# Optimization experiments

Hardware: AMD Instinct MI355X
Metric: run time of the kernel (lower is better)

The kernel has to match this reference:

```python
import jax, jax.numpy as jnp
import numpy as np

N = 50000          # nodes
E = 800000         # edges
D_IN = 96          # node_encoding_length
D = 128            # hidden_encoding_length (args.node_encoding)
B = 512            # graphs in batch
MPNN_STEPS = 4
S2S_STEPS = 3


def setup_inputs() -> dict:
    key = jax.random.key(0)
    ks = jax.random.split(key, 12)
    x = jax.random.normal(ks[0], (N, D_IN), dtype=jnp.float32)
    edge_index = jax.random.randint(ks[1], (2, E), 0, N, dtype=jnp.int64)
    batch = jnp.sort(jax.random.randint(ks[2], (N,), 0, B, dtype=jnp.int64))
    s_in = 1.0 / np.sqrt(D_IN)
    W_in = jax.random.uniform(ks[3], (D, D_IN), jnp.float32, -s_in, s_in)
    b_in = jax.random.uniform(ks[4], (D,), jnp.float32, -s_in, s_in)
    s_l = 1.0 / np.sqrt(D)
    W_ih = jax.random.uniform(ks[5], (4 * D, 2 * D), jnp.float32, -s_l, s_l)
    W_hh = jax.random.uniform(ks[6], (4 * D, D), jnp.float32, -s_l, s_l)
    b_ih = jax.random.uniform(ks[7], (4 * D,), jnp.float32, -s_l, s_l)
    b_hh = jax.random.uniform(ks[8], (4 * D,), jnp.float32, -s_l, s_l)
    s_p = 1.0 / np.sqrt(2 * D)
    W_pred = jax.random.uniform(ks[9], (1, 2 * D), jnp.float32, -s_p, s_p)
    b_pred = jax.random.uniform(ks[10], (1,), jnp.float32, -s_p, s_p)
    return {"x": x, "edge_index": edge_index, "batch": batch,
            "W_in": W_in, "b_in": b_in, "W_ih": W_ih, "W_hh": W_hh,
            "b_ih": b_ih, "b_hh": b_hh, "W_pred": W_pred, "b_pred": b_pred}


def _forward(x, edge_index, batch, W_in, b_in, W_ih, W_hh, b_ih, b_hh, W_pred, b_pred):
    # input layer + relu
    h = jax.nn.relu(x @ W_in.T + b_in)                      # [N, D]
    src, dst = edge_index[0], edge_index[1]
    # precompute in-degree for mean aggregation (clamped to 1 like scatter-mean)
    deg = jax.ops.segment_sum(jnp.ones((E,), h.dtype), dst, num_segments=N)
    deg = jnp.maximum(deg, 1.0)[:, None]                    # [N, 1]
    # MPNN: gather x_j at src, mean-aggregate at dst, update x=(x+msg)/2
    for _ in range(MPNN_STEPS):
        msg = jax.ops.segment_sum(h[src], dst, num_segments=N) / deg
        h = (h + msg) * 0.5
    # Set2Set readout
    d = h.shape[1]
    q_star = jnp.zeros((B, 2 * d), h.dtype)
    hh = jnp.zeros((B, d), h.dtype)
    cc = jnp.zeros((B, d), h.dtype)
    for _ in range(S2S_STEPS):
        gates = q_star @ W_ih.T + b_ih + hh @ W_hh.T + b_hh  # [B, 4d]
        i_g, f_g, g_g, o_g = jnp.split(gates, 4, axis=-1)
        cc = jax.nn.sigmoid(f_g) * cc + jax.nn.sigmoid(i_g) * jnp.tanh(g_g)
        hh = jax.nn.sigmoid(o_g) * jnp.tanh(cc)
        q = hh                                               # [B, d]
        e = jnp.sum(h * q[batch], axis=-1)                   # [N]
        e_max = jax.ops.segment_max(e, batch, num_segments=B)
        a = jnp.exp(e - e_max[batch])
        a_sum = jax.ops.segment_sum(a, batch, num_segments=B)
        a = a / (a_sum[batch] + 1e-16)
        r = jax.ops.segment_sum(a[:, None] * h, batch, num_segments=B)  # [B, d]
        q_star = jnp.concatenate([q, r], axis=-1)
    return q_star @ W_pred.T + b_pred                        # [B, 1]


def reference(x, edge_index, batch, W_in, b_in, W_ih, W_hh, b_ih, b_hh, W_pred, b_pred):
    return _forward(x, edge_index, batch, W_in, b_in, W_ih, W_hh, b_ih, b_hh, W_pred, b_pred)
```

## Files before the change

### kernel.cpp

```cpp
#include <hip/hip_runtime.h>
#include <math.h>
#include <float.h>

#define N_NODES 50000
#define N_EDGES 800000
#define D_INP   96
#define D_HID   128
#define N_B     512
#define CAP     64
#define XS_LD   100

typedef __attribute__((ext_vector_type(4))) _Float16 half4;
typedef __attribute__((ext_vector_type(8))) _Float16 half8;

__global__ __launch_bounds__(256) void k_ingemm_prep(
        const float* __restrict__ x,
        const float* __restrict__ W_in,
        const float* __restrict__ b_in,
        const float* __restrict__ W_ih,
        const float* __restrict__ W_hh,
        const int* __restrict__ batch,
        _Float16* __restrict__ h16,
        float* __restrict__ Wt2,
        int* __restrict__ cnt,
        int* __restrict__ seg_ptr) {
    int gid = (blockIdx.y * gridDim.x + blockIdx.x) * 256 + threadIdx.x;
    if (gid < N_NODES) {
        cnt[gid] = 0;
        int n = gid;
        int bc = batch[n];
        int bp = (n == 0) ? -1 : batch[n - 1];
        for (int b = bp + 1; b <= bc; b++) seg_ptr[b] = n;
        if (n == N_NODES - 1)
            for (int b = bc + 1; b <= N_B; b++) seg_ptr[b] = N_NODES;
    }
    if (gid < 256 * 512) {
        int k = gid / 512, g = gid % 512;
        float v = W_ih[g * 256 + k];
        if (k < 128) v += W_hh[g * 128 + k];
        Wt2[gid] = v;
    }

    __shared__ __align__(16) float xs[64 * XS_LD];
    __shared__ __align__(16) float ws[96 * 64];
    int n0 = blockIdx.x * 64;
    int d0 = blockIdx.y * 64;
    int tid = threadIdx.x;
    for (int j = tid; j < 64 * 96 / 4; j += 256) {
        int row = (j * 4) / 96, col = (j * 4) % 96;
        int node = n0 + row;
        float4 v = make_float4(0.f, 0.f, 0.f, 0.f);
        if (node < N_NODES) v = *(const float4*)&x[(size_t)node * 96 + col];
        *(float4*)&xs[row * XS_LD + col] = v;
    }
    for (int i = tid; i < 96 * 64; i += 256) {
        int k = i >> 6, dd = i & 63;
        ws[i] = W_in[(size_t)(d0 + dd) * 96 + k];
    }
    __syncthreads();
    int tn = tid / 16;
    int td = tid % 16;
    float acc[4][4] = {};
    for (int k0 = 0; k0 < 96; k0 += 4) {
        float4 w0 = *(float4*)&ws[(k0 + 0) * 64 + td * 4];
        float4 w1 = *(float4*)&ws[(k0 + 1) * 64 + td * 4];
        float4 w2 = *(float4*)&ws[(k0 + 2) * 64 + td * 4];
        float4 w3 = *(float4*)&ws[(k0 + 3) * 64 + td * 4];
#pragma unroll
        for (int j = 0; j < 4; j++) {
            float4 xv = *(float4*)&xs[(tn * 4 + j) * XS_LD + k0];
            acc[j][0] += xv.x * w0.x + xv.y * w1.x + xv.z * w2.x + xv.w * w3.x;
            acc[j][1] += xv.x * w0.y + xv.y * w1.y + xv.z * w2.y + xv.w * w3.y;
            acc[j][2] += xv.x * w0.z + xv.y * w1.z + xv.z * w2.z + xv.w * w3.z;
            acc[j][3] += xv.x * w0.w + xv.y * w1.w + xv.z * w2.w + xv.w * w3.w;
        }
    }
    float4 bb = *(const float4*)&b_in[d0 + td * 4];
#pragma unroll
    for (int j = 0; j < 4; j++) {
        int node = n0 + tn * 4 + j;
        if (node < N_NODES) {
            half4 s;
            s.x = (_Float16)fmaxf(acc[j][0] + bb.x, 0.f);
            s.y = (_Float16)fmaxf(acc[j][1] + bb.y, 0.f);
            s.z = (_Float16)fmaxf(acc[j][2] + bb.z, 0.f);
            s.w = (_Float16)fmaxf(acc[j][3] + bb.w, 0.f);
            *(half4*)&h16[(size_t)node * D_HID + d0 + td * 4] = s;
        }
    }
}

__global__ void k_bucket8(const int* __restrict__ src, const int* __restrict__ dst,
                          int* __restrict__ cnt, unsigned short* __restrict__ esrc) {
    int chunk = blockIdx.x >> 3;
    int part  = blockIdx.x & 7;
    int e = chunk * 256 + threadIdx.x;
    if (e < N_EDGES) {
        int d = dst[e];
        if ((d & 7) == part) {
            int p = atomicAdd(&cnt[d], 1);
            if (p < CAP) esrc[(size_t)d * CAP + p] = (unsigned short)src[e];
        }
    }
}

__global__ __launch_bounds__(256) void k_mpnn(const _Float16* __restrict__ hin16,
                                              _Float16* __restrict__ hout16,
                                              const int* __restrict__ cnt,
                                              const unsigned short* __restrict__ esrc) {
    int g = threadIdx.x >> 4;
    int l = threadIdx.x & 15;
    int n = blockIdx.x * 16 + g;
    if (n >= N_NODES) return;
    int deg = cnt[n];
    int len = min(deg, CAP);
    const unsigned short* row = &esrc[(size_t)n * CAP];
    float a0[8] = {}, a1[8] = {}, a2[8] = {}, a3[8] = {};
    int i = 0;
    for (; i + 4 <= len; i += 4) {
        int e0 = row[i + 0];
        int e1 = row[i + 1];
        int e2 = row[i + 2];
        int e3 = row[i + 3];
        half8 v0 = *(const half8*)&hin16[(size_t)e0 * 128 + l * 8];
        half8 v1 = *(const half8*)&hin16[(size_t)e1 * 128 + l * 8];
        half8 v2 = *(const half8*)&hin16[(size_t)e2 * 128 + l * 8];
        half8 v3 = *(const half8*)&hin16[(size_t)e3 * 128 + l * 8];
#pragma unroll
        for (int c = 0; c < 8; c++) {
            a0[c] += (float)v0[c];
            a1[c] += (float)v1[c];
            a2[c] += (float)v2[c];
            a3[c] += (float)v3[c];
        }
    }
    for (; i < len; i++) {
        int e0 = row[i];
        half8 v0 = *(const half8*)&hin16[(size_t)e0 * 128 + l * 8];
#pragma unroll
        for (int c = 0; c < 8; c++) a0[c] += (float)v0[c];
    }
#pragma unroll
    for (int c = 0; c < 8; c++) a0[c] += a1[c] + a2[c] + a3[c];
    float invd = 1.0f / (float)max(deg, 1);
    half8 sv = *(const half8*)&hin16[(size_t)n * 128 + l * 8];
    half8 s;
#pragma unroll
    for (int c = 0; c < 8; c++)
        s[c] = (_Float16)(((float)sv[c] + a0[c] * invd) * 0.5f);
    *(half8*)&hout16[(size_t)n * 128 + l * 8] = s;
}

__device__ __forceinline__ float sigmoidf_(float v) { return 1.0f / (1.0f + expf(-v)); }

__global__ __launch_bounds__(1024) void k_s2s2(const float* __restrict__ Wt2,
                                               const float* __restrict__ b_ih,
                                               const float* __restrict__ b_hh,
                                               const _Float16* __restrict__ h16,
                                               const int* __restrict__ seg_ptr,
                                               const float* __restrict__ W_pred,
                                               const float* __restrict__ b_pred,
                                               float* __restrict__ out) {
    __shared__ __align__(16) float in_s[2 * 256];
    __shared__ __align__(16) float c_s[2 * 128];
    __shared__ __align__(16) float bias_s[512];
    __shared__ __align__(16) float gpart_s[2][2][512];
    __shared__ float smax_s[2][16];
    __shared__ float ssum_s[2][16];
    __shared__ __align__(16) float sr_s[2][16][128];

    int t = threadIdx.x;
    if (t < 512) {
        in_s[t] = 0.f;
        bias_s[t] = b_ih[t] + b_hh[t];
    }
    if (t < 256) c_s[t] = 0.f;

    int gate = t & 511;
    int kh   = t >> 9;
    int row  = t >> 9;
    int loc  = t & 511;
    int gq   = loc >> 5;
    int l    = t & 31;
    int b    = blockIdx.x * 2 + row;
    int s0 = seg_ptr[b], s1 = seg_ptr[b + 1];

    for (int step = 0; step < 3; step++) {
        __syncthreads();
        {
            float acc0 = 0.f, acc1 = 0.f;
            int k0 = kh * 128;
#pragma unroll 8
            for (int k = k0; k < k0 + 128; k++) {
                float w = Wt2[k * 512 + gate];
                acc0 += in_s[k] * w;
                acc1 += in_s[256 + k] * w;
            }
            gpart_s[kh][0][gate] = acc0;
            gpart_s[kh][1][gate] = acc1;
        }
        __syncthreads();
        if (t < 256) {
            int r2 = t >> 7, ff = t & 127;
            float ig = gpart_s[0][r2][ff]       + gpart_s[1][r2][ff]       + bias_s[ff];
            float fg = gpart_s[0][r2][128 + ff] + gpart_s[1][r2][128 + ff] + bias_s[128 + ff];
            float gg = gpart_s[0][r2][256 + ff] + gpart_s[1][r2][256 + ff] + bias_s[256 + ff];
            float og = gpart_s[0][r2][384 + ff] + gpart_s[1][r2][384 + ff] + bias_s[384 + ff];
            float c = sigmoidf_(fg) * c_s[r2 * 128 + ff] + sigmoidf_(ig) * tanhf(gg);
            c_s[r2 * 128 + ff] = c;
            in_s[r2 * 256 + ff] = sigmoidf_(og) * tanhf(c);
        }
        __syncthreads();
        float4 q = *(float4*)&in_s[row * 256 + l * 4];
        float Ma = -INFINITY, sa = 0.f;
        float Mb = -INFINITY, sb = 0.f;
        float4 ra = make_float4(0.f, 0.f, 0.f, 0.f);
        float4 rb = make_float4(0.f, 0.f, 0.f, 0.f);
        for (int n = s0 + gq; n < s1; n += 32) {
            {
                half4 h4 = *(const half4*)&h16[(size_t)n * 128 + l * 4];
                float4 hv = make_float4((float)h4.x, (float)h4.y, (float)h4.z, (float)h4.w);
                float d = hv.x * q.x + hv.y * q.y + hv.z * q.z + hv.w * q.w;
                for (int m = 16; m >= 1; m >>= 1) d += __shfl_xor(d, m, 64);
                float nM = fmaxf(Ma, d);
                float sc = expf(Ma - nM);
                float a = expf(d - nM);
                sa = sa * sc + a;
                ra.x = ra.x * sc + a * hv.x;
                ra.y = ra.y * sc + a * hv.y;
                ra.z = ra.z * sc + a * hv.z;
                ra.w = ra.w * sc + a * hv.w;
                Ma = nM;
            }
            int n2 = n + 16;
            if (n2 < s1) {
                half4 h4 = *(const half4*)&h16[(size_t)n2 * 128 + l * 4];
                float4 hv = make_float4((float)h4.x, (float)h4.y, (float)h4.z, (float)h4.w);
                float d = hv.x * q.x + hv.y * q.y + hv.z * q.z + hv.w * q.w;
                for (int m = 16; m >= 1; m >>= 1) d += __shfl_xor(d, m, 64);
                float nM = fmaxf(Mb, d);
                float sc = expf(Mb - nM);
                float a = expf(d - nM);
                sb = sb * sc + a;
                rb.x = rb.x * sc + a * hv.x;
                rb.y = rb.y * sc + a * hv.y;
                rb.z = rb.z * sc + a * hv.z;
                rb.w = rb.w * sc + a * hv.w;
                Mb = nM;
            }
        }
        float M = fmaxf(Ma, Mb);
        float wa = (Ma > -INFINITY) ? expf(Ma - M) : 0.f;
        float wb = (Mb > -INFINITY) ? expf(Mb - M) : 0.f;
        float asum = sa * wa + sb * wb;
        float4 racc;
        racc.x = ra.x * wa + rb.x * wb;
        racc.y = ra.y * wa + rb.y * wb;
        racc.z = ra.z * wa + rb.z * wb;
        racc.w = ra.w * wa + rb.w * wb;
        if (l == 0) { smax_s[row][gq] = M; ssum_s[row][gq] = asum; }
        *(float4*)&sr_s[row][gq][l * 4] = racc;
        __syncthreads();
        if (gq == 0) {
            float Mx = -INFINITY;
#pragma unroll
            for (int i = 0; i < 16; i++) Mx = fmaxf(Mx, smax_s[row][i]);
            float4 o = make_float4(0.f, 0.f, 0.f, 0.f);
            if (Mx > -INFINITY) {
                float tot = 0.f;
                float4 osum = make_float4(0.f, 0.f, 0.f, 0.f);
#pragma unroll
                for (int i = 0; i < 16; i++) {
                    float wi = expf(smax_s[row][i] - Mx);
                    tot += ssum_s[row][i] * wi;
                    float4 ri = *(float4*)&sr_s[row][i][l * 4];
                    osum.x += ri.x * wi; osum.y += ri.y * wi;
                    osum.z += ri.z * wi; osum.w += ri.w * wi;
                }
                float inv = 1.0f / (tot + 1e-16f);
                o.x = osum.x * inv; o.y = osum.y * inv;
                o.z = osum.z * inv; o.w = osum.w * inv;
            }
            *(float4*)&in_s[row * 256 + 128 + l * 4] = o;
            if (step == 2) {
                float4 wq = *(const float4*)&W_pred[l * 4];
                float4 wr = *(const float4*)&W_pred[128 + l * 4];
                float d = q.x * wq.x + q.y * wq.y + q.z * wq.z + q.w * wq.w
                        + o.x * wr.x + o.y * wr.y + o.z * wr.z + o.w * wr.w;
                for (int m = 16; m >= 1; m >>= 1) d += __shfl_xor(d, m, 64);
                if (l == 0) out[b] = d + b_pred[0];
            }
        }
    }
}

extern "C" void kernel_launch(void* const* d_in, const int* in_sizes, int n_in,
                              void* d_out, int out_size, void* d_ws, size_t ws_size,
                              hipStream_t stream) {
    const float* x      = (const float*)d_in[0];
    const int*   edge   = (const int*)d_in[1];
    const int*   batch  = (const int*)d_in[2];
    const float* W_in   = (const float*)d_in[3];
    const float* b_in   = (const float*)d_in[4];
    const float* W_ih   = (const float*)d_in[5];
    const float* W_hh   = (const float*)d_in[6];
    const float* b_ih   = (const float*)d_in[7];
    const float* b_hh   = (const float*)d_in[8];
    const float* W_pred = (const float*)d_in[9];
    const float* b_pred = (const float*)d_in[10];
    float* out = (float*)d_out;

    const int* src = edge;
    const int* dst = edge + N_EDGES;

    float* f = (float*)d_ws;
    _Float16* g0 = (_Float16*)f;          f += (size_t)N_NODES * D_HID / 2;
    _Float16* g1 = (_Float16*)f;          f += (size_t)N_NODES * D_HID / 2;
    float* Wt2   = f;                     f += 256 * 512;
    int* ip = (int*)f;
    int* cnt     = ip;                    ip += N_NODES;
    int* seg_ptr = ip;                    ip += N_B + 1 + 3;
    unsigned short* esrc = (unsigned short*)ip;

    k_ingemm_prep<<<dim3((N_NODES + 63) / 64, 2), 256, 0, stream>>>(
        x, W_in, b_in, W_ih, W_hh, batch, g0, Wt2, cnt, seg_ptr);

    k_bucket8<<<((N_EDGES + 255) / 256) * 8, 256, 0, stream>>>(src, dst, cnt, esrc);

    int mb = (N_NODES + 15) / 16;
    k_mpnn<<<mb, 256, 0, stream>>>(g0, g1, cnt, esrc);
    k_mpnn<<<mb, 256, 0, stream>>>(g1, g0, cnt, esrc);
    k_mpnn<<<mb, 256, 0, stream>>>(g0, g1, cnt, esrc);
    k_mpnn<<<mb, 256, 0, stream>>>(g1, g0, cnt, esrc);

    k_s2s2<<<N_B / 2, 1024, 0, stream>>>(Wt2, b_ih, b_hh, g0, seg_ptr,
                                         W_pred, b_pred, out);
}
```

Baseline: 321.6 us.

## Fuse final MPNN step into Set2Set kernel with per-graph LDS node cache

```diff
diff --git a/kernel.cpp b/kernel.cpp
--- a/kernel.cpp
+++ b/kernel.cpp
@@ -9,43 +9,37 @@
 #define N_B     512
 #define CAP     64
 #define XS_LD   100
+#define HLN     160
+#define TAILCAP 64
 
 typedef __attribute__((ext_vector_type(4))) _Float16 half4;
 typedef __attribute__((ext_vector_type(8))) _Float16 half8;
 
-__global__ __launch_bounds__(256) void k_ingemm_prep(
-        const float* __restrict__ x,
-        const float* __restrict__ W_in,
-        const float* __restrict__ b_in,
-        const float* __restrict__ W_ih,
-        const float* __restrict__ W_hh,
-        const int* __restrict__ batch,
-        _Float16* __restrict__ h16,
-        float* __restrict__ Wt2,
-        int* __restrict__ cnt,
-        int* __restrict__ seg_ptr) {
+__global__ __launch_bounds__(256) void k_ingemm(const float* __restrict__ x,
+                                                const float* __restrict__ W_in,
+                                                const float* __restrict__ b_in,
+                                                _Float16* __restrict__ h16,
+                                                int* __restrict__ cnt) {
     int gid = (blockIdx.y * gridDim.x + blockIdx.x) * 256 + threadIdx.x;
-    if (gid < N_NODES) {
-        cnt[gid] = 0;
-        int n = gid;
-        int bc = batch[n];
-        int bp = (n == 0) ? -1 : batch[n - 1];
-        for (int b = bp + 1; b <= bc; b++) seg_ptr[b] = n;
-        if (n == N_NODES - 1)
-            for (int b = bc + 1; b <= N_B; b++) seg_ptr[b] = N_NODES;
-    }
-    if (gid < 256 * 512) {
-        int k = gid / 512, g = gid % 512;
-        float v = W_ih[g * 256 + k];
-        if (k < 128) v += W_hh[g * 128 + k];
-        Wt2[gid] = v;
-    }
+    if (gid < N_NODES) cnt[gid] = 0;
 
     __shared__ __align__(16) float xs[64 * XS_LD];
     __shared__ __align__(16) float ws[96 * 64];
     int n0 = blockIdx.x * 64;
     int d0 = blockIdx.y * 64;
     int tid = threadIdx.x;
+
+    for (int i = tid; i < 64 * 24; i += 256) {
+        int row = i / 24, c4 = i % 24;
+        float4 v = *(const float4*)&W_in[(size_t)(d0 + row) * 96 + c4 * 4];
+        *(float4*)&xs[row * XS_LD + c4 * 4] = v;
+    }
+    __syncthreads();
+    for (int i = tid; i < 96 * 64; i += 256) {
+        int k = i >> 6, dd = i & 63;
+        ws[i] = xs[dd * XS_LD + k];
+    }
+    __syncthreads();
     for (int j = tid; j < 64 * 96 / 4; j += 256) {
         int row = (j * 4) / 96, col = (j * 4) % 96;
         int node = n0 + row;
@@ -53,11 +47,8 @@
         if (node < N_NODES) v = *(const float4*)&x[(size_t)node * 96 + col];
         *(float4*)&xs[row * XS_LD + col] = v;
     }
-    for (int i = tid; i < 96 * 64; i += 256) {
-        int k = i >> 6, dd = i & 63;
-        ws[i] = W_in[(size_t)(d0 + dd) * 96 + k];
-    }
     __syncthreads();
+
     int tn = tid / 16;
     int td = tid % 16;
     float acc[4][4] = {};
@@ -91,7 +82,26 @@
 }
 
 __global__ void k_bucket8(const int* __restrict__ src, const int* __restrict__ dst,
-                          int* __restrict__ cnt, unsigned short* __restrict__ esrc) {
+                          const int* __restrict__ batch,
+                          const float* __restrict__ W_ih,
+                          const float* __restrict__ W_hh,
+                          int* __restrict__ cnt, unsigned short* __restrict__ esrc,
+                          int* __restrict__ seg_ptr, float* __restrict__ Wt2) {
+    int gid = blockIdx.x * 256 + threadIdx.x;
+    if (gid < N_NODES) {
+        int n = gid;
+        int bc = batch[n];
+        int bp = (n == 0) ? -1 : batch[n - 1];
+        for (int b = bp + 1; b <= bc; b++) seg_ptr[b] = n;
+        if (n == N_NODES - 1)
+            for (int b = bc + 1; b <= N_B; b++) seg_ptr[b] = N_NODES;
+    }
+    if (gid < 256 * 512) {
+        int k = gid / 512, g = gid % 512;
+        float v = W_ih[g * 256 + k];
+        if (k < 128) v += W_hh[g * 128 + k];
+        Wt2[gid] = v;
+    }
     int chunk = blockIdx.x >> 3;
     int part  = blockIdx.x & 7;
     int e = chunk * 256 + threadIdx.x;
@@ -153,144 +163,160 @@
 
 __device__ __forceinline__ float sigmoidf_(float v) { return 1.0f / (1.0f + expf(-v)); }
 
-__global__ __launch_bounds__(1024) void k_s2s2(const float* __restrict__ Wt2,
-                                               const float* __restrict__ b_ih,
-                                               const float* __restrict__ b_hh,
-                                               const _Float16* __restrict__ h16,
-                                               const int* __restrict__ seg_ptr,
-                                               const float* __restrict__ W_pred,
-                                               const float* __restrict__ b_pred,
-                                               float* __restrict__ out) {
-    __shared__ __align__(16) float in_s[2 * 256];
-    __shared__ __align__(16) float c_s[2 * 128];
+__global__ __launch_bounds__(512) void k_s2s3(const float* __restrict__ Wt2,
+                                              const float* __restrict__ b_ih,
+                                              const float* __restrict__ b_hh,
+                                              const _Float16* __restrict__ h3,
+                                              const int* __restrict__ cnt,
+                                              const unsigned short* __restrict__ esrc,
+                                              const int* __restrict__ seg_ptr,
+                                              const float* __restrict__ W_pred,
+                                              const float* __restrict__ b_pred,
+                                              _Float16* __restrict__ tail,
+                                              float* __restrict__ out) {
+    __shared__ __align__(16) _Float16 hl[HLN * 128];
+    __shared__ __align__(16) float sr_s[32][128];
+    __shared__ __align__(16) float gates_s[512];
+    __shared__ __align__(16) float in_s[256];
+    __shared__ __align__(16) float c_s[128];
     __shared__ __align__(16) float bias_s[512];
-    __shared__ __align__(16) float gpart_s[2][2][512];
-    __shared__ float smax_s[2][16];
-    __shared__ float ssum_s[2][16];
-    __shared__ __align__(16) float sr_s[2][16][128];
+    __shared__ float smax_s[32];
+    __shared__ float ssum_s[32];
+    __shared__ float red_s[128];
 
     int t = threadIdx.x;
-    if (t < 512) {
-        in_s[t] = 0.f;
-        bias_s[t] = b_ih[t] + b_hh[t];
-    }
-    if (t < 256) c_s[t] = 0.f;
-
-    int gate = t & 511;
-    int kh   = t >> 9;
-    int row  = t >> 9;
-    int loc  = t & 511;
-    int gq   = loc >> 5;
-    int l    = t & 31;
-    int b    = blockIdx.x * 2 + row;
+    int b = blockIdx.x;
+    if (t < 256) in_s[t] = 0.f;
+    if (t < 128) c_s[t] = 0.f;
+    bias_s[t] = b_ih[t] + b_hh[t];
+
     int s0 = seg_ptr[b], s1 = seg_ptr[b + 1];
+    int len = s1 - s0;
+    if (len > HLN + TAILCAP) len = HLN + TAILCAP;
+
+    int grp = t >> 4;
+    int lane = t & 15;
+
+    for (int nl = grp; nl < len; nl += 32) {
+        int n = s0 + nl;
+        int deg = cnt[n];
+        int ln = min(deg, CAP);
+        const unsigned short* row = &esrc[(size_t)n * CAP];
+        float a0[8] = {}, a1[8] = {}, a2[8] = {}, a3[8] = {};
+        int i = 0;
+        for (; i + 4 <= ln; i += 4) {
+            int e0 = row[i + 0];
+            int e1 = row[i + 1];
+            int e2 = row[i + 2];
+            int e3 = row[i + 3];
+            half8 v0 = *(const half8*)&h3[(size_t)e0 * 128 + lane * 8];
+            half8 v1 = *(const half8*)&h3[(size_t)e1 * 128 + lane * 8];
+            half8 v2 = *(const half8*)&h3[(size_t)e2 * 128 + lane * 8];
+            half8 v3 = *(const half8*)&h3[(size_t)e3 * 128 + lane * 8];
+#pragma unroll
+            for (int c = 0; c < 8; c++) {
+                a0[c] += (float)v0[c];
+                a1[c] += (float)v1[c];
+                a2[c] += (float)v2[c];
+                a3[c] += (float)v3[c];
+            }
+        }
+        for (; i < ln; i++) {
+            int e0 = row[i];
+            half8 v0 = *(const half8*)&h3[(size_t)e0 * 128 + lane * 8];
+#pragma unroll
+            for (int c = 0; c < 8; c++) a0[c] += (float)v0[c];
+        }
+#pragma unroll
+        for (int c = 0; c < 8; c++) a0[c] += a1[c] + a2[c] + a3[c];
+        float invd = 1.0f / (float)max(deg, 1);
+        half8 sv = *(const half8*)&h3[(size_t)n * 128 + lane * 8];
+        half8 o16;
+#pragma unroll
+        for (int c = 0; c < 8; c++)
+            o16[c] = (_Float16)(((float)sv[c] + a0[c] * invd) * 0.5f);
+        if (nl < HLN)
+            *(half8*)&hl[nl * 128 + lane * 8] = o16;
+        else
+            *(half8*)&tail[((size_t)b * TAILCAP + (nl - HLN)) * 128 + lane * 8] = o16;
+    }
+    __syncthreads();
 
     for (int step = 0; step < 3; step++) {
+        {
+            float acc = 0.f;
+#pragma unroll 8
+            for (int k = 0; k < 256; k++)
+                acc += in_s[k] * Wt2[k * 512 + t];
+            gates_s[t] = acc + bias_s[t];
+        }
         __syncthreads();
-        {
-            float acc0 = 0.f, acc1 = 0.f;
-            int k0 = kh * 128;
-#pragma unroll 8
-            for (int k = k0; k < k0 + 128; k++) {
-                float w = Wt2[k * 512 + gate];
-                acc0 += in_s[k] * w;
-                acc1 += in_s[256 + k] * w;
+        if (t < 128) {
+            float ig = gates_s[t];
+            float fg = gates_s[128 + t];
+            float gg = gates_s[256 + t];
+            float og = gates_s[384 + t];
+            float c = sigmoidf_(fg) * c_s[t] + sigmoidf_(ig) * tanhf(gg);
+            c_s[t] = c;
+            in_s[t] = sigmoidf_(og) * tanhf(c);
+        }
+        __syncthreads();
+        float qr[8];
+#pragma unroll
+        for (int c = 0; c < 8; c++) qr[c] = in_s[lane * 8 + c];
+        float M = -INFINITY, asum = 0.f;
+        float racc[8] = {};
+        for (int nl = grp; nl < len; nl += 32) {
+            half8 hv;
+            if (nl < HLN) hv = *(const half8*)&hl[nl * 128 + lane * 8];
+            else hv = *(const half8*)&tail[((size_t)b * TAILCAP + (nl - HLN)) * 128 + lane * 8];
+            float hf[8];
+#pragma unroll
+            for (int c = 0; c < 8; c++) hf[c] = (float)hv[c];
+            float d = 0.f;
+#pragma unroll
+            for (int c = 0; c < 8; c++) d += qr[c] * hf[c];
+            d += __shfl_xor(d, 8, 64);
+            d += __shfl_xor(d, 4, 64);
+            d += __shfl_xor(d, 2, 64);
+            d += __shfl_xor(d, 1, 64);
+            float nM = fmaxf(M, d);
+            float sc = expf(M - nM);
+            float a = expf(d - nM);
+            asum = asum * sc + a;
+#pragma unroll
+            for (int c = 0; c < 8; c++) racc[c] = racc[c] * sc + a * hf[c];
+            M = nM;
+        }
+        if (lane == 0) { smax_s[grp] = M; ssum_s[grp] = asum; }
+#pragma unroll
+        for (int c = 0; c < 8; c++) sr_s[grp][lane * 8 + c] = racc[c];
+        __syncthreads();
+        if (t < 128) {
+            float Mx = -INFINITY;
+#pragma unroll
+            for (int g = 0; g < 32; g++) Mx = fmaxf(Mx, smax_s[g]);
+            float o = 0.f;
+            if (Mx > -INFINITY) {
+                float tot = 0.f, osum = 0.f;
+#pragma unroll
+                for (int g = 0; g < 32; g++) {
+                    float w = expf(smax_s[g] - Mx);
+                    tot += ssum_s[g] * w;
+                    osum += sr_s[g][t] * w;
+                }
+                o = osum / (tot + 1e-16f);
             }
-            gpart_s[kh][0][gate] = acc0;
-            gpart_s[kh][1][gate] = acc1;
+            in_s[128 + t] = o;
+            if (step == 2)
+                red_s[t] = in_s[t] * W_pred[t] + o * W_pred[128 + t];
         }
         __syncthreads();
-        if (t < 256) {
-            int r2 = t >> 7, ff = t & 127;
-            float ig = gpart_s[0][r2][ff]       + gpart_s[1][r2][ff]       + bias_s[ff];
-            float fg = gpart_s[0][r2][128 + ff] + gpart_s[1][r2][128 + ff] + bias_s[128 + ff];
-            float gg = gpart_s[0][r2][256 + ff] + gpart_s[1][r2][256 + ff] + bias_s[256 + ff];
-            float og = gpart_s[0][r2][384 + ff] + gpart_s[1][r2][384 + ff] + bias_s[384 + ff];
-            float c = sigmoidf_(fg) * c_s[r2 * 128 + ff] + sigmoidf_(ig) * tanhf(gg);
-            c_s[r2 * 128 + ff] = c;
-            in_s[r2 * 256 + ff] = sigmoidf_(og) * tanhf(c);
-        }
-        __syncthreads();
-        float4 q = *(float4*)&in_s[row * 256 + l * 4];
-        float Ma = -INFINITY, sa = 0.f;
-        float Mb = -INFINITY, sb = 0.f;
-        float4 ra = make_float4(0.f, 0.f, 0.f, 0.f);
-        float4 rb = make_float4(0.f, 0.f, 0.f, 0.f);
-        for (int n = s0 + gq; n < s1; n += 32) {
-            {
-                half4 h4 = *(const half4*)&h16[(size_t)n * 128 + l * 4];
-                float4 hv = make_float4((float)h4.x, (float)h4.y, (float)h4.z, (float)h4.w);
-                float d = hv.x * q.x + hv.y * q.y + hv.z * q.z + hv.w * q.w;
-                for (int m = 16; m >= 1; m >>= 1) d += __shfl_xor(d, m, 64);
-                float nM = fmaxf(Ma, d);
-                float sc = expf(Ma - nM);
-                float a = expf(d - nM);
-                sa = sa * sc + a;
-                ra.x = ra.x * sc + a * hv.x;
-                ra.y = ra.y * sc + a * hv.y;
-                ra.z = ra.z * sc + a * hv.z;
-                ra.w = ra.w * sc + a * hv.w;
-                Ma = nM;
-            }
-            int n2 = n + 16;
-            if (n2 < s1) {
-                half4 h4 = *(const half4*)&h16[(size_t)n2 * 128 + l * 4];
-                float4 hv = make_float4((float)h4.x, (float)h4.y, (float)h4.z, (float)h4.w);
-                float d = hv.x * q.x + hv.y * q.y + hv.z * q.z + hv.w * q.w;
-                for (int m = 16; m >= 1; m >>= 1) d += __shfl_xor(d, m, 64);
-                float nM = fmaxf(Mb, d);
-                float sc = expf(Mb - nM);
-                float a = expf(d - nM);
-                sb = sb * sc + a;
-                rb.x = rb.x * sc + a * hv.x;
-                rb.y = rb.y * sc + a * hv.y;
-                rb.z = rb.z * sc + a * hv.z;
-                rb.w = rb.w * sc + a * hv.w;
-                Mb = nM;
-            }
-        }
-        float M = fmaxf(Ma, Mb);
-        float wa = (Ma > -INFINITY) ? expf(Ma - M) : 0.f;
-        float wb = (Mb > -INFINITY) ? expf(Mb - M) : 0.f;
-        float asum = sa * wa + sb * wb;
-        float4 racc;
-        racc.x = ra.x * wa + rb.x * wb;
-        racc.y = ra.y * wa + rb.y * wb;
-        racc.z = ra.z * wa + rb.z * wb;
-        racc.w = ra.w * wa + rb.w * wb;
-        if (l == 0) { smax_s[row][gq] = M; ssum_s[row][gq] = asum; }
-        *(float4*)&sr_s[row][gq][l * 4] = racc;
-        __syncthreads();
-        if (gq == 0) {
-            float Mx = -INFINITY;
-#pragma unroll
-            for (int i = 0; i < 16; i++) Mx = fmaxf(Mx, smax_s[row][i]);
-            float4 o = make_float4(0.f, 0.f, 0.f, 0.f);
-            if (Mx > -INFINITY) {
-                float tot = 0.f;
-                float4 osum = make_float4(0.f, 0.f, 0.f, 0.f);
-#pragma unroll
-                for (int i = 0; i < 16; i++) {
-                    float wi = expf(smax_s[row][i] - Mx);
-                    tot += ssum_s[row][i] * wi;
-                    float4 ri = *(float4*)&sr_s[row][i][l * 4];
-                    osum.x += ri.x * wi; osum.y += ri.y * wi;
-                    osum.z += ri.z * wi; osum.w += ri.w * wi;
-                }
-                float inv = 1.0f / (tot + 1e-16f);
-                o.x = osum.x * inv; o.y = osum.y * inv;
-                o.z = osum.z * inv; o.w = osum.w * inv;
-            }
-            *(float4*)&in_s[row * 256 + 128 + l * 4] = o;
-            if (step == 2) {
-                float4 wq = *(const float4*)&W_pred[l * 4];
-                float4 wr = *(const float4*)&W_pred[128 + l * 4];
-                float d = q.x * wq.x + q.y * wq.y + q.z * wq.z + q.w * wq.w
-                        + o.x * wr.x + o.y * wr.y + o.z * wr.z + o.w * wr.w;
-                for (int m = 16; m >= 1; m >>= 1) d += __shfl_xor(d, m, 64);
-                if (l == 0) out[b] = d + b_pred[0];
-            }
-        }
+    }
+    if (t < 64) {
+        float s = red_s[t] + red_s[t + 64];
+        for (int m = 32; m >= 1; m >>= 1) s += __shfl_xor(s, m, 64);
+        if (t == 0) out[b] = s + b_pred[0];
     }
 }
 
@@ -316,23 +342,23 @@
     float* f = (float*)d_ws;
     _Float16* g0 = (_Float16*)f;          f += (size_t)N_NODES * D_HID / 2;
     _Float16* g1 = (_Float16*)f;          f += (size_t)N_NODES * D_HID / 2;
+    _Float16* tail = (_Float16*)f;        f += (size_t)N_B * TAILCAP * D_HID / 2;
     float* Wt2   = f;                     f += 256 * 512;
     int* ip = (int*)f;
     int* cnt     = ip;                    ip += N_NODES;
     int* seg_ptr = ip;                    ip += N_B + 1 + 3;
     unsigned short* esrc = (unsigned short*)ip;
 
-    k_ingemm_prep<<<dim3((N_NODES + 63) / 64, 2), 256, 0, stream>>>(
-        x, W_in, b_in, W_ih, W_hh, batch, g0, Wt2, cnt, seg_ptr);
-
-    k_bucket8<<<((N_EDGES + 255) / 256) * 8, 256, 0, stream>>>(src, dst, cnt, esrc);
+    k_ingemm<<<dim3((N_NODES + 63) / 64, 2), 256, 0, stream>>>(x, W_in, b_in, g0, cnt);
+
+    k_bucket8<<<((N_EDGES + 255) / 256) * 8, 256, 0, stream>>>(
+        src, dst, batch, W_ih, W_hh, cnt, esrc, seg_ptr, Wt2);
 
     int mb = (N_NODES + 15) / 16;
     k_mpnn<<<mb, 256, 0, stream>>>(g0, g1, cnt, esrc);
     k_mpnn<<<mb, 256, 0, stream>>>(g1, g0, cnt, esrc);
     k_mpnn<<<mb, 256, 0, stream>>>(g0, g1, cnt, esrc);
-    k_mpnn<<<mb, 256, 0, stream>>>(g1, g0, cnt, esrc);
-
-    k_s2s2<<<N_B / 2, 1024, 0, stream>>>(Wt2, b_ih, b_hh, g0, seg_ptr,
-                                         W_pred, b_pred, out);
-}
+
+    k_s2s3<<<N_B, 512, 0, stream>>>(Wt2, b_ih, b_hh, g1, cnt, esrc, seg_ptr,
+                                    W_pred, b_pred, tail, out);
+}
```

Result: no change. 318.1 us (-1.1%).
